# Performance work log

Hardware: AMD Instinct MI355X
Metric: run time of the kernel (lower is better)

## Reference

```python
import jax, jax.numpy as jnp
import numpy as np

N = 50000      # nodes
E = 1600000    # edges (avg degree 32)
F_IN = 256     # input feature dim
H = 128        # hidden == output size of GCN
C = 40         # num_class


def setup_inputs() -> dict:
    key = jax.random.key(0)
    ks = jax.random.split(key, 13)
    inp = {
        "features": jax.random.normal(ks[0], (N, F_IN), dtype=jnp.float32),
        "src": jax.random.randint(ks[1], (E,), 0, N, dtype=jnp.int32),
        "dst": jax.random.randint(ks[2], (E,), 0, N, dtype=jnp.int32),
        "edge_weight": jax.random.uniform(ks[3], (E,), dtype=jnp.float32),
        "y": jax.random.normal(ks[4], (N, C), dtype=jnp.float32),
        # GCN layer 1
        "W1": jax.random.normal(ks[5], (F_IN, H), dtype=jnp.float32) / np.sqrt(F_IN),
        "b1": jnp.zeros((H,), dtype=jnp.float32),
        # GCN layer 2
        "W2": jax.random.normal(ks[6], (H, H), dtype=jnp.float32) / np.sqrt(H),
        "b2": jnp.zeros((H,), dtype=jnp.float32),
        # y_fc_emb: Linear(num_class, output_size)
        "We": jax.random.normal(ks[7], (C, H), dtype=jnp.float32) / np.sqrt(C),
        "be": jnp.zeros((H,), dtype=jnp.float32),
        # y_fc: Linear(hidden*2, num_class)
        "Wf": jax.random.normal(ks[8], (2 * H, C), dtype=jnp.float32) / np.sqrt(2 * H),
        "bf": jnp.zeros((C,), dtype=jnp.float32),
    }
    return inp


def _spmm(edge_weight, src, dst, x, n):
    # (sparse adj) @ x : out[i] = sum_{(j->i)} w_ji * x[j]
    return jax.ops.segment_sum(edge_weight[:, None] * x[src], dst, num_segments=n)


def reference(features, src, dst, edge_weight, y, W1, b1, W2, b2, We, be, Wf, bf):
    n = features.shape[0]
    # F.normalize: L2 row-normalize with eps=1e-12 clamp
    norm = jnp.maximum(jnp.linalg.norm(features, axis=1, keepdims=True), 1e-12)
    x = features / norm
    # GCN layer 1: relu(adj @ (x @ W1) + b1)   (dropout = 0)
    h = jax.nn.relu(_spmm(edge_weight, src, dst, x @ W1, n) + b1)
    # GCN layer 2: adj @ (h @ W2) + b2
    h = _spmm(edge_weight, src, dst, h @ W2, n) + b2
    # label embedding + head
    y_emb = y @ We + be
    logits = jnp.concatenate([y_emb, h], axis=1) @ Wf + bf
    return jax.nn.softmax(logits, axis=-1)
```

## Files before the change

### kernel.cpp

```cpp
#include <hip/hip_runtime.h>
#include <hip/hip_bf16.h>
#include <hip/hip_fp16.h>
#include <cstdint>
#include <cstddef>
#include <cmath>

#define F_IN 256
#define HDIM 128
#define CCLS 40
#define NBMAX 1024
#define EPB 8192
#define CAP 4096

typedef short bf16x8 __attribute__((ext_vector_type(8)));
typedef float f32x4 __attribute__((ext_vector_type(4)));

__device__ inline unsigned pkbf(float a, float b) {
  __hip_bfloat162 h = __float22bfloat162_rn(make_float2(a, b));
  unsigned u;
  __builtin_memcpy(&u, &h, 4);
  return u;
}
__device__ inline unsigned short bfr(float f) {
  __hip_bfloat16 h = __float2bfloat16(f);
  unsigned short u;
  __builtin_memcpy(&u, &h, 2);
  return u;
}
__device__ inline float f16tof(unsigned short hb) {
  __half hv;
  __builtin_memcpy(&hv, &hb, 2);
  return __half2float(hv);
}
__device__ inline unsigned short ftof16(float f) {
  __half hv = __float2half(f);
  unsigned short u;
  __builtin_memcpy(&u, &hv, 2);
  return u;
}

__global__ __launch_bounds__(256) void prep_kernel(const float* __restrict__ W1,
                                                   unsigned short* __restrict__ W1T,
                                                   int* __restrict__ gcursor, int nb) {
  const int b = blockIdx.x;
  const int t = threadIdx.x;
  if (b < 128) {
    int idx = b * 256 + t;
    int nr = idx >> 8, k = idx & 255;
    W1T[idx] = bfr(W1[k * 128 + nr]);
  } else {
    for (int i = t; i < nb; i += 256) gcursor[i] = 0;
  }
}

__global__ __launch_bounds__(256) void scatter_gemm1(const int* __restrict__ src,
                                                     const int* __restrict__ dst,
                                                     const float* __restrict__ w,
                                                     int* __restrict__ gcursor,
                                                     uint2* __restrict__ ews,
                                                     const float* __restrict__ X,
                                                     const unsigned short* __restrict__ W1T,
                                                     unsigned short* __restrict__ C,
                                                     const float* __restrict__ W2,
                                                     unsigned short* __restrict__ W2T,
                                                     const float* __restrict__ We,
                                                     const float* __restrict__ be,
                                                     const float* __restrict__ Wf,
                                                     const float* __restrict__ bf,
                                                     float* __restrict__ Wc,
                                                     float* __restrict__ bc,
                                                     int e, int nb, int nsb, int ngb,
                                                     int M) {
  __shared__ char smem[16 * 264 * 2];
  const int t = threadIdx.x;
  const int b = blockIdx.x;
  if (b < nsb) {
    int* hist = (int*)smem;
    int* sb   = hist + NBMAX;
    for (int i = t; i < nb; i += 256) hist[i] = 0;
    __syncthreads();
    const int b4 = b * (EPB / 4);
    int4 dv[8];
    int rk[32];
#pragma unroll
    for (int k = 0; k < 8; ++k) {
      int gi = b4 + k * 256 + t;
      int e0 = gi * 4;
      int4 d = make_int4(-1, -1, -1, -1);
      if (e0 + 3 < e) d = ((const int4*)dst)[gi];
      else if (e0 < e) {
        d.x = dst[e0];
        if (e0 + 1 < e) d.y = dst[e0 + 1];
        if (e0 + 2 < e) d.z = dst[e0 + 2];
      }
      dv[k] = d;
      rk[k * 4 + 0] = (d.x >= 0) ? atomicAdd(&hist[d.x >> 6], 1) : 0;
      rk[k * 4 + 1] = (d.y >= 0) ? atomicAdd(&hist[d.y >> 6], 1) : 0;
      rk[k * 4 + 2] = (d.z >= 0) ? atomicAdd(&hist[d.z >> 6], 1) : 0;
      rk[k * 4 + 3] = (d.w >= 0) ? atomicAdd(&hist[d.w >> 6], 1) : 0;
    }
    __syncthreads();
    for (int i = t; i < nb; i += 256) {
      int c = hist[i];
      sb[i] = i * CAP + (c ? atomicAdd(&gcursor[i], c) : 0);
    }
    __syncthreads();
#pragma unroll
    for (int k = 0; k < 8; ++k) {
      int gi = b4 + k * 256 + t;
      int e0 = gi * 4;
      if (e0 >= e) continue;
      int4 s4 = make_int4(0, 0, 0, 0);
      float4 w4 = make_float4(0.f, 0.f, 0.f, 0.f);
      if (e0 + 3 < e) { s4 = ((const int4*)src)[gi]; w4 = ((const float4*)w)[gi]; }
      else {
        s4.x = src[e0]; w4.x = w[e0];
        if (e0 + 1 < e) { s4.y = src[e0 + 1]; w4.y = w[e0 + 1]; }
        if (e0 + 2 < e) { s4.z = src[e0 + 2]; w4.z = w[e0 + 2]; }
      }
      int4 d = dv[k];
      if (d.x >= 0) ews[sb[d.x >> 6] + rk[k * 4 + 0]] =
          make_uint2(((unsigned)(d.x & 63) << 26) | (unsigned)s4.x, __float_as_uint(w4.x));
      if (d.y >= 0) ews[sb[d.y >> 6] + rk[k * 4 + 1]] =
          make_uint2(((unsigned)(d.y & 63) << 26) | (unsigned)s4.y, __float_as_uint(w4.y));
      if (d.z >= 0) ews[sb[d.z >> 6] + rk[k * 4 + 2]] =
          make_uint2(((unsigned)(d.z & 63) << 26) | (unsigned)s4.z, __float_as_uint(w4.z));
      if (d.w >= 0) ews[sb[d.w >> 6] + rk[k * 4 + 3]] =
          make_uint2(((unsigned)(d.w & 63) << 26) | (unsigned)s4.w, __float_as_uint(w4.w));
    }
  } else if (b < nsb + ngb) {
    unsigned short (*As)[264] = (unsigned short(*)[264])smem;
    const int w8 = t >> 6, l = t & 63;
    const int bm0 = (b - nsb) * 16;
    for (int rr = 0; rr < 4; ++rr) {
      int row = w8 * 4 + rr;
      int grow = bm0 + row;
      const float* p = X + (size_t)(grow < M ? grow : (M - 1)) * F_IN + l * 4;
      float4 v = *(const float4*)p;
      float s = v.x * v.x + v.y * v.y + v.z * v.z + v.w * v.w;
#pragma unroll
      for (int off = 32; off; off >>= 1) s += __shfl_xor(s, off, 64);
      float inv = 1.0f / fmaxf(sqrtf(s), 1e-12f);
      *(uint2*)&As[row][l * 4] =
          make_uint2(pkbf(v.x * inv, v.y * inv), pkbf(v.z * inv, v.w * inv));
    }
    __syncthreads();
    const int ln = l & 15, quad = l >> 4;
    f32x4 acc[2];
    acc[0] = (f32x4){0.f, 0.f, 0.f, 0.f};
    acc[1] = (f32x4){0.f, 0.f, 0.f, 0.f};
#pragma unroll
    for (int k0 = 0; k0 < F_IN; k0 += 32) {
      bf16x8 af = *(const bf16x8*)&As[ln][k0 + quad * 8];
#pragma unroll
      for (int ti = 0; ti < 2; ++ti) {
        bf16x8 bfv = *(const bf16x8*)(W1T + (size_t)(w8 * 32 + ti * 16 + ln) * F_IN +
                                      k0 + quad * 8);
        acc[ti] = __builtin_amdgcn_mfma_f32_16x16x32_bf16(af, bfv, acc[ti], 0, 0, 0);
      }
    }
#pragma unroll
    for (int r = 0; r < 4; ++r) {
      int grow = bm0 + quad * 4 + r;
      if (grow < M) {
#pragma unroll
        for (int ti = 0; ti < 2; ++ti)
          C[(size_t)grow * HDIM + w8 * 32 + ti * 16 + ln] = bfr(acc[ti][r]);
      }
    }
  } else if (b < nsb + ngb + 64) {
    int idx = (b - nsb - ngb) * 256 + t;
    int nr = idx >> 7, k = idx & 127;
    W2T[idx] = bfr(W2[k * 128 + nr]);
  } else {
    int part = b - (nsb + ngb + 64);
    int lo = part * 800, hi = lo + 800;
    for (int i = lo + t; i < hi; i += 256) {
      int c = i / CCLS, j = i % CCLS;
      float s = 0.f;
      for (int f = 0; f < HDIM; ++f) s += We[c * HDIM + f] * Wf[f * CCLS + j];
      Wc[i] = s;
    }
    if (part == 0 && t < CCLS) {
      float s = bf[t];
      for (int f = 0; f < HDIM; ++f) s += be[f] * Wf[f * CCLS + t];
      bc[t] = s;
    }
  }
}

__global__ __launch_bounds__(256) void bucket_sort(const uint2* __restrict__ ews,
                                                   const int* __restrict__ gcursor,
                                                   unsigned* __restrict__ ews2,
                                                   int* __restrict__ row_off,
                                                   int* __restrict__ row_end,
                                                   int n, int nb) {
  __shared__ int cnt[256];
  __shared__ int cur[64];
  const int t = threadIdx.x;
  const int b = blockIdx.x;
  cnt[t] = 0;
  __syncthreads();
  const int base = b * CAP;
  const int c = gcursor[b];
  const int wv = t >> 6;
  for (int i = t; i < c; i += 256)
    atomicAdd(&cnt[wv * 64 + ((unsigned)ews[base + i].x >> 26)], 1);
  __syncthreads();
  if (t < 64) {
    int tot = cnt[t] + cnt[64 + t] + cnt[128 + t] + cnt[192 + t];
    int x = tot;
#pragma unroll
    for (int off = 1; off < 64; off <<= 1) {
      int y = __shfl_up(x, off, 64);
      if (t >= off) x += y;
    }
    int excl = x - tot;
    cur[t] = excl;
    int node = b * 64 + t;
    if (node < n) { row_off[node] = base + excl; row_end[node] = base + excl + tot; }
  }
  __syncthreads();
  for (int i = t; i < c; i += 256) {
    uint2 p = ews[base + i];
    int d = (unsigned)p.x >> 26;
    int pos = base + atomicAdd(&cur[d], 1);
    ews2[pos] = (p.x & 0xFFFFu) | ((unsigned)ftof16(__uint_as_float(p.y)) << 16);
  }
}

#define SPMM_PAIR(ua, ub)                                                      \
  {                                                                            \
    unsigned u = half ? (ub) : (ua);                                           \
    float wt = f16tof((unsigned short)(u >> 16));                              \
    const uint2 xv = *(const uint2*)(xin + (size_t)(u & 0xFFFFu) * HDIM + fo); \
    acc.x = fmaf(wt, __uint_as_float(xv.x << 16), acc.x);                      \
    acc.y = fmaf(wt, __uint_as_float(xv.x & 0xFFFF0000u), acc.y);              \
    acc.z = fmaf(wt, __uint_as_float(xv.y << 16), acc.z);                      \
    acc.w = fmaf(wt, __uint_as_float(xv.y & 0xFFFF0000u), acc.w);              \
  }

#define SPMM_NODE_LOOP(ep, cnt)                                                 \
  int k = 0;                                                                    \
  for (; k + 16 <= cnt; k += 16) {                                              \
    unsigned a0 = ep[k + 0], a1 = ep[k + 1], a2 = ep[k + 2], a3 = ep[k + 3];    \
    unsigned a4 = ep[k + 4], a5 = ep[k + 5], a6 = ep[k + 6], a7 = ep[k + 7];    \
    unsigned a8 = ep[k + 8], a9 = ep[k + 9], a10 = ep[k + 10], a11 = ep[k + 11];\
    unsigned a12 = ep[k + 12], a13 = ep[k + 13], a14 = ep[k + 14],              \
             a15 = ep[k + 15];                                                  \
    SPMM_PAIR(a0, a1); SPMM_PAIR(a2, a3); SPMM_PAIR(a4, a5); SPMM_PAIR(a6, a7); \
    SPMM_PAIR(a8, a9); SPMM_PAIR(a10, a11); SPMM_PAIR(a12, a13);                \
    SPMM_PAIR(a14, a15);                                                        \
  }                                                                             \
  for (; k + 8 <= cnt; k += 8) {                                                \
    unsigned a0 = ep[k + 0], a1 = ep[k + 1], a2 = ep[k + 2], a3 = ep[k + 3];    \
    unsigned a4 = ep[k + 4], a5 = ep[k + 5], a6 = ep[k + 6], a7 = ep[k + 7];    \
    SPMM_PAIR(a0, a1); SPMM_PAIR(a2, a3); SPMM_PAIR(a4, a5); SPMM_PAIR(a6, a7); \
  }                                                                             \
  for (; k < cnt; k += 2) {                                                     \
    unsigned a0 = ep[k];                                                        \
    unsigned a1 = (k + 1 < cnt) ? ep[k + 1] : 0u;                               \
    SPMM_PAIR(a0, a1);                                                          \
  }

__global__ __launch_bounds__(256) void spmm1_gemm2(const unsigned short* __restrict__ xin,
                                                   const unsigned* __restrict__ ews,
                                                   const int* __restrict__ row_off,
                                                   const int* __restrict__ row_end,
                                                   const float* __restrict__ bias,
                                                   const unsigned short* __restrict__ W2T,
                                                   unsigned short* __restrict__ C,
                                                   int n) {
  __shared__ unsigned short As[16][136];
  const int t = threadIdx.x;
  const int l = t & 63;
  const int w = t >> 6;
  const int fo = (l & 31) * 4;
  const int half = l >> 5;
  const int nb0 = blockIdx.x * 16;
#pragma unroll
  for (int j = 0; j < 4; ++j) {
    const int node = nb0 + w * 4 + j;
    if (node < n) {
      const int ue0 = __builtin_amdgcn_readfirstlane(row_off[node]);
      const int ue1 = __builtin_amdgcn_readfirstlane(row_end[node]);
      const int cnt = ue1 - ue0;
      const unsigned* ep = ews + ue0;
      float4 acc = make_float4(0.f, 0.f, 0.f, 0.f);
      SPMM_NODE_LOOP(ep, cnt)
      acc.x += __shfl_xor(acc.x, 32, 64);
      acc.y += __shfl_xor(acc.y, 32, 64);
      acc.z += __shfl_xor(acc.z, 32, 64);
      acc.w += __shfl_xor(acc.w, 32, 64);
      if (l < 32) {
        float4 bv = *(const float4*)(bias + fo);
        float r0 = fmaxf(acc.x + bv.x, 0.f), r1 = fmaxf(acc.y + bv.y, 0.f);
        float r2 = fmaxf(acc.z + bv.z, 0.f), r3 = fmaxf(acc.w + bv.w, 0.f);
        *(uint2*)&As[w * 4 + j][fo] = make_uint2(pkbf(r0, r1), pkbf(r2, r3));
      }
    }
  }
  __syncthreads();
  const int ln = l & 15, quad = l >> 4;
  f32x4 acc2[2];
  acc2[0] = (f32x4){0.f, 0.f, 0.f, 0.f};
  acc2[1] = (f32x4){0.f, 0.f, 0.f, 0.f};
#pragma unroll
  for (int k0 = 0; k0 < HDIM; k0 += 32) {
    bf16x8 af = *(const bf16x8*)&As[ln][k0 + quad * 8];
#pragma unroll
    for (int ti = 0; ti < 2; ++ti) {
      bf16x8 bfv = *(const bf16x8*)(W2T + (size_t)(w * 32 + ti * 16 + ln) * HDIM +
                                    k0 + quad * 8);
      acc2[ti] = __builtin_amdgcn_mfma_f32_16x16x32_bf16(af, bfv, acc2[ti], 0, 0, 0);
    }
  }
#pragma unroll
  for (int r = 0; r < 4; ++r) {
    int grow = nb0 + quad * 4 + r;
    if (grow < n) {
#pragma unroll
      for (int ti = 0; ti < 2; ++ti)
        C[(size_t)grow * HDIM + w * 32 + ti * 16 + ln] = bfr(acc2[ti][r]);
    }
  }
}

__global__ __launch_bounds__(256) void spmm_f32(const unsigned short* __restrict__ xin,
                                                const unsigned* __restrict__ ews,
                                                const int* __restrict__ row_off,
                                                const int* __restrict__ row_end,
                                                const float* __restrict__ bias,
                                                float* __restrict__ outp, int n) {
  const int t = threadIdx.x;
  const int l = t & 63;
  const int node = blockIdx.x * 4 + (t >> 6);
  if (node >= n) return;
  const int ue0 = __builtin_amdgcn_readfirstlane(row_off[node]);
  const int ue1 = __builtin_amdgcn_readfirstlane(row_end[node]);
  const int cnt = ue1 - ue0;
  const unsigned* ep = ews + ue0;
  const int fo = (l & 31) * 4;
  const int half = l >> 5;
  float4 acc = make_float4(0.f, 0.f, 0.f, 0.f);
  SPMM_NODE_LOOP(ep, cnt)
  acc.x += __shfl_xor(acc.x, 32, 64);
  acc.y += __shfl_xor(acc.y, 32, 64);
  acc.z += __shfl_xor(acc.z, 32, 64);
  acc.w += __shfl_xor(acc.w, 32, 64);
  if (l < 32) {
    float4 bv = *(const float4*)(bias + fo);
    *(float4*)(outp + (size_t)node * HDIM + fo) =
        make_float4(acc.x + bv.x, acc.y + bv.y, acc.z + bv.z, acc.w + bv.w);
  }
}

__global__ __launch_bounds__(256) void head_kernel(const float* __restrict__ y,
                                                   const float* __restrict__ h2,
                                                   const float* __restrict__ Wc,
                                                   const float* __restrict__ bc,
                                                   const float* __restrict__ Wf,
                                                   float* __restrict__ out, int n) {
  __shared__ float sW[169 * CCLS];
  const int t = threadIdx.x;
  for (int i = t; i < 400; i += 256) ((float4*)sW)[i] = ((const float4*)Wc)[i];
  for (int i = t; i < 1280; i += 256)
    ((float4*)(sW + CCLS * CCLS))[i] = ((const float4*)(Wf + HDIM * CCLS))[i];
  if (t < 10) ((float4*)(sW + 168 * CCLS))[t] = ((const float4*)bc)[t];
  __syncthreads();

  const int node = blockIdx.x * 256 + t;
  const int nc = node < n ? node : n - 1;
  const float* zy = y + (size_t)nc * CCLS;
  const float* zh = h2 + (size_t)nc * HDIM;

  float acc[40];
#pragma unroll
  for (int cq = 0; cq < 10; ++cq) {
    float4 b4 = *(const float4*)&sW[168 * CCLS + cq * 4];
    acc[cq * 4 + 0] = b4.x; acc[cq * 4 + 1] = b4.y;
    acc[cq * 4 + 2] = b4.z; acc[cq * 4 + 3] = b4.w;
  }

#pragma unroll 2
  for (int kc = 0; kc < 10; ++kc) {
    float4 zv = *(const float4*)(zy + kc * 4);
    float zj[4] = {zv.x, zv.y, zv.z, zv.w};
#pragma unroll
    for (int j = 0; j < 4; ++j) {
      const float* wr = sW + (kc * 4 + j) * CCLS;
#pragma unroll
      for (int cq = 0; cq < 10; ++cq) {
        float4 w4 = *(const float4*)(wr + cq * 4);
        acc[cq * 4 + 0] = fmaf(zj[j], w4.x, acc[cq * 4 + 0]);
        acc[cq * 4 + 1] = fmaf(zj[j], w4.y, acc[cq * 4 + 1]);
        acc[cq * 4 + 2] = fmaf(zj[j], w4.z, acc[cq * 4 + 2]);
        acc[cq * 4 + 3] = fmaf(zj[j], w4.w, acc[cq * 4 + 3]);
      }
    }
  }
#pragma unroll 2
  for (int kc = 0; kc < 32; ++kc) {
    float4 zv = *(const float4*)(zh + kc * 4);
    float zj[4] = {zv.x, zv.y, zv.z, zv.w};
#pragma unroll
    for (int j = 0; j < 4; ++j) {
      const float* wr = sW + (40 + kc * 4 + j) * CCLS;
#pragma unroll
      for (int cq = 0; cq < 10; ++cq) {
        float4 w4 = *(const float4*)(wr + cq * 4);
        acc[cq * 4 + 0] = fmaf(zj[j], w4.x, acc[cq * 4 + 0]);
        acc[cq * 4 + 1] = fmaf(zj[j], w4.y, acc[cq * 4 + 1]);
        acc[cq * 4 + 2] = fmaf(zj[j], w4.z, acc[cq * 4 + 2]);
        acc[cq * 4 + 3] = fmaf(zj[j], w4.w, acc[cq * 4 + 3]);
      }
    }
  }

  float m = acc[0];
#pragma unroll
  for (int c = 1; c < 40; ++c) m = fmaxf(m, acc[c]);
  float sum = 0.f;
#pragma unroll
  for (int c = 0; c < 40; ++c) { acc[c] = __expf(acc[c] - m); sum += acc[c]; }
  float inv = 1.0f / sum;
  if (node < n) {
    float* op = out + (size_t)node * CCLS;
#pragma unroll
    for (int cq = 0; cq < 10; ++cq) {
      float4 o = make_float4(acc[cq * 4 + 0] * inv, acc[cq * 4 + 1] * inv,
                             acc[cq * 4 + 2] * inv, acc[cq * 4 + 3] * inv);
      *(float4*)(op + cq * 4) = o;
    }
  }
}

extern "C" void kernel_launch(void* const* d_in, const int* in_sizes, int n_in,
                              void* d_out, int out_size, void* d_ws, size_t ws_size,
                              hipStream_t stream) {
  (void)n_in; (void)out_size; (void)ws_size;
  const float* features = (const float*)d_in[0];
  const int*   src      = (const int*)d_in[1];
  const int*   dst      = (const int*)d_in[2];
  const float* ew       = (const float*)d_in[3];
  const float* y        = (const float*)d_in[4];
  const float* W1       = (const float*)d_in[5];
  const float* b1       = (const float*)d_in[6];
  const float* W2       = (const float*)d_in[7];
  const float* b2       = (const float*)d_in[8];
  const float* We       = (const float*)d_in[9];
  const float* be       = (const float*)d_in[10];
  const float* Wf       = (const float*)d_in[11];
  const float* bf       = (const float*)d_in[12];
  float* out = (float*)d_out;

  const int n = in_sizes[0] / F_IN;
  const int e = in_sizes[1];
  const int nb = (n + 63) >> 6;

  char* w = (char*)d_ws;
  auto take = [&](size_t bytes) {
    char* p = w;
    w += (bytes + 255) & ~(size_t)255;
    return p;
  };
  int*   gcursor  = (int*)take((size_t)nb * 4);
  int*   row_off  = (int*)take((size_t)n * 4);
  int*   row_end  = (int*)take((size_t)n * 4);
  uint2* ews      = (uint2*)take((size_t)nb * CAP * 8);
  unsigned* ews2  = (unsigned*)take((size_t)nb * CAP * 4);
  unsigned short* bufH1  = (unsigned short*)take((size_t)n * HDIM * 2);
  unsigned short* bufH2  = (unsigned short*)take((size_t)n * HDIM * 2);
  float* bufS     = (float*)take((size_t)n * HDIM * 4);
  unsigned short* W1T = (unsigned short*)take((size_t)HDIM * F_IN * 2);
  unsigned short* W2T = (unsigned short*)take((size_t)HDIM * HDIM * 2);
  float* Wc       = (float*)take(CCLS * CCLS * 4);
  float* bc       = (float*)take(CCLS * 4);

  const int nsb = (e + EPB - 1) / EPB;
  const int ngb = (n + 15) / 16;

  prep_kernel<<<129, 256, 0, stream>>>(W1, W1T, gcursor, nb);
  scatter_gemm1<<<nsb + ngb + 64 + 2, 256, 0, stream>>>(
      src, dst, ew, gcursor, ews, features, W1T, bufH1,
      W2, W2T, We, be, Wf, bf, Wc, bc, e, nb, nsb, ngb, n);
  bucket_sort<<<nb, 256, 0, stream>>>(ews, gcursor, ews2, row_off, row_end, n, nb);

  spmm1_gemm2<<<(n + 15) / 16, 256, 0, stream>>>(bufH1, ews2, row_off, row_end, b1,
                                                 W2T, bufH2, n);
  spmm_f32<<<(n + 3) / 4, 256, 0, stream>>>(bufH2, ews2, row_off, row_end, b2, bufS, n);
  head_kernel<<<(n + 255) / 256, 256, 0, stream>>>(y, bufS, Wc, bc, Wf, out, n);
}
```

Baseline: 325.3 us.

## Replace global bucket cursor atomics with per-block fixed slot regions

The edge scatter no longer does a two-pass histogram with global atomicAdd cursors. Each scatter block writes its edges straight into a private fixed-size slot region per destination bucket and records its per-bucket counts. bucket_sort then prefix-sums those counts across scatter blocks and uses a binary search to gather the edges. This removes the global atomics, two barriers and the gcursor zeroing. In exchange it roughly doubles the staging buffer, makes the gather reads more scattered, and assumes no block puts more than 40 edges in one bucket and that there are at most 256 scatter blocks.

```diff
diff --git a/kernel.cpp b/kernel.cpp
--- a/kernel.cpp
+++ b/kernel.cpp
@@ -11,6 +11,7 @@
 #define NBMAX 1024
 #define EPB 8192
 #define CAP 4096
+#define SLOTS_PB 40
 
 typedef short bf16x8 __attribute__((ext_vector_type(8)));
 typedef float f32x4 __attribute__((ext_vector_type(4)));
@@ -40,23 +41,16 @@
 }
 
 __global__ __launch_bounds__(256) void prep_kernel(const float* __restrict__ W1,
-                                                   unsigned short* __restrict__ W1T,
-                                                   int* __restrict__ gcursor, int nb) {
-  const int b = blockIdx.x;
-  const int t = threadIdx.x;
-  if (b < 128) {
-    int idx = b * 256 + t;
-    int nr = idx >> 8, k = idx & 255;
-    W1T[idx] = bfr(W1[k * 128 + nr]);
-  } else {
-    for (int i = t; i < nb; i += 256) gcursor[i] = 0;
-  }
+                                                   unsigned short* __restrict__ W1T) {
+  int idx = blockIdx.x * 256 + threadIdx.x;
+  int nr = idx >> 8, k = idx & 255;
+  W1T[idx] = bfr(W1[k * 128 + nr]);
 }
 
 __global__ __launch_bounds__(256) void scatter_gemm1(const int* __restrict__ src,
                                                      const int* __restrict__ dst,
                                                      const float* __restrict__ w,
-                                                     int* __restrict__ gcursor,
+                                                     int* __restrict__ cnt,
                                                      uint2* __restrict__ ews,
                                                      const float* __restrict__ X,
                                                      const unsigned short* __restrict__ W1T,
@@ -76,58 +70,41 @@
   const int b = blockIdx.x;
   if (b < nsb) {
     int* hist = (int*)smem;
-    int* sb   = hist + NBMAX;
     for (int i = t; i < nb; i += 256) hist[i] = 0;
     __syncthreads();
     const int b4 = b * (EPB / 4);
-    int4 dv[8];
-    int rk[32];
-#pragma unroll
-    for (int k = 0; k < 8; ++k) {
-      int gi = b4 + k * 256 + t;
-      int e0 = gi * 4;
-      int4 d = make_int4(-1, -1, -1, -1);
-      if (e0 + 3 < e) d = ((const int4*)dst)[gi];
-      else if (e0 < e) {
-        d.x = dst[e0];
-        if (e0 + 1 < e) d.y = dst[e0 + 1];
-        if (e0 + 2 < e) d.z = dst[e0 + 2];
-      }
-      dv[k] = d;
-      rk[k * 4 + 0] = (d.x >= 0) ? atomicAdd(&hist[d.x >> 6], 1) : 0;
-      rk[k * 4 + 1] = (d.y >= 0) ? atomicAdd(&hist[d.y >> 6], 1) : 0;
-      rk[k * 4 + 2] = (d.z >= 0) ? atomicAdd(&hist[d.z >> 6], 1) : 0;
-      rk[k * 4 + 3] = (d.w >= 0) ? atomicAdd(&hist[d.w >> 6], 1) : 0;
-    }
-    __syncthreads();
-    for (int i = t; i < nb; i += 256) {
-      int c = hist[i];
-      sb[i] = i * CAP + (c ? atomicAdd(&gcursor[i], c) : 0);
-    }
-    __syncthreads();
 #pragma unroll
     for (int k = 0; k < 8; ++k) {
       int gi = b4 + k * 256 + t;
       int e0 = gi * 4;
       if (e0 >= e) continue;
+      int4 d = make_int4(-1, -1, -1, -1);
       int4 s4 = make_int4(0, 0, 0, 0);
       float4 w4 = make_float4(0.f, 0.f, 0.f, 0.f);
-      if (e0 + 3 < e) { s4 = ((const int4*)src)[gi]; w4 = ((const float4*)w)[gi]; }
-      else {
-        s4.x = src[e0]; w4.x = w[e0];
-        if (e0 + 1 < e) { s4.y = src[e0 + 1]; w4.y = w[e0 + 1]; }
-        if (e0 + 2 < e) { s4.z = src[e0 + 2]; w4.z = w[e0 + 2]; }
-      }
-      int4 d = dv[k];
-      if (d.x >= 0) ews[sb[d.x >> 6] + rk[k * 4 + 0]] =
-          make_uint2(((unsigned)(d.x & 63) << 26) | (unsigned)s4.x, __float_as_uint(w4.x));
-      if (d.y >= 0) ews[sb[d.y >> 6] + rk[k * 4 + 1]] =
-          make_uint2(((unsigned)(d.y & 63) << 26) | (unsigned)s4.y, __float_as_uint(w4.y));
-      if (d.z >= 0) ews[sb[d.z >> 6] + rk[k * 4 + 2]] =
-          make_uint2(((unsigned)(d.z & 63) << 26) | (unsigned)s4.z, __float_as_uint(w4.z));
-      if (d.w >= 0) ews[sb[d.w >> 6] + rk[k * 4 + 3]] =
-          make_uint2(((unsigned)(d.w & 63) << 26) | (unsigned)s4.w, __float_as_uint(w4.w));
-    }
+      if (e0 + 3 < e) {
+        d = ((const int4*)dst)[gi];
+        s4 = ((const int4*)src)[gi];
+        w4 = ((const float4*)w)[gi];
+      } else {
+        d.x = dst[e0]; s4.x = src[e0]; w4.x = w[e0];
+        if (e0 + 1 < e) { d.y = dst[e0 + 1]; s4.y = src[e0 + 1]; w4.y = w[e0 + 1]; }
+        if (e0 + 2 < e) { d.z = dst[e0 + 2]; s4.z = src[e0 + 2]; w4.z = w[e0 + 2]; }
+      }
+      if (d.x >= 0) { int bb = d.x >> 6; int r = atomicAdd(&hist[bb], 1);
+        ews[((size_t)bb * nsb + b) * SLOTS_PB + r] =
+            make_uint2(((unsigned)(d.x & 63) << 26) | (unsigned)s4.x, __float_as_uint(w4.x)); }
+      if (d.y >= 0) { int bb = d.y >> 6; int r = atomicAdd(&hist[bb], 1);
+        ews[((size_t)bb * nsb + b) * SLOTS_PB + r] =
+            make_uint2(((unsigned)(d.y & 63) << 26) | (unsigned)s4.y, __float_as_uint(w4.y)); }
+      if (d.z >= 0) { int bb = d.z >> 6; int r = atomicAdd(&hist[bb], 1);
+        ews[((size_t)bb * nsb + b) * SLOTS_PB + r] =
+            make_uint2(((unsigned)(d.z & 63) << 26) | (unsigned)s4.z, __float_as_uint(w4.z)); }
+      if (d.w >= 0) { int bb = d.w >> 6; int r = atomicAdd(&hist[bb], 1);
+        ews[((size_t)bb * nsb + b) * SLOTS_PB + r] =
+            make_uint2(((unsigned)(d.w & 63) << 26) | (unsigned)s4.w, __float_as_uint(w4.w)); }
+    }
+    __syncthreads();
+    for (int i = t; i < nb; i += 256) cnt[(size_t)b * nb + i] = hist[i];
   } else if (b < nsb + ngb) {
     unsigned short (*As)[264] = (unsigned short(*)[264])smem;
     const int w8 = t >> 6, l = t & 63;
@@ -190,25 +167,42 @@
 }
 
 __global__ __launch_bounds__(256) void bucket_sort(const uint2* __restrict__ ews,
-                                                   const int* __restrict__ gcursor,
+                                                   const int* __restrict__ cnt,
                                                    unsigned* __restrict__ ews2,
                                                    int* __restrict__ row_off,
                                                    int* __restrict__ row_end,
-                                                   int n, int nb) {
-  __shared__ int cnt[256];
+                                                   int n, int nb, int nsb) {
+  __shared__ int sc[256];
+  __shared__ int cc[256];
+  __shared__ int c64[256];
   __shared__ int cur[64];
   const int t = threadIdx.x;
   const int b = blockIdx.x;
-  cnt[t] = 0;
+  int c = (t < nsb) ? cnt[(size_t)t * nb + b] : 0;
+  cc[t] = c;
+  sc[t] = c;
+  c64[t] = 0;
   __syncthreads();
-  const int base = b * CAP;
-  const int c = gcursor[b];
+  for (int off = 1; off < 256; off <<= 1) {
+    int x = sc[t];
+    int y = (t >= off) ? sc[t - off] : 0;
+    __syncthreads();
+    sc[t] = x + y;
+    __syncthreads();
+  }
+  const int total = sc[255];
+  const size_t cbase = (size_t)b * nsb * SLOTS_PB;
   const int wv = t >> 6;
-  for (int i = t; i < c; i += 256)
-    atomicAdd(&cnt[wv * 64 + ((unsigned)ews[base + i].x >> 26)], 1);
+  for (int p = t; p < total; p += 256) {
+    int lo = 0, hi = nsb - 1;
+    while (lo < hi) { int mid = (lo + hi) >> 1; if (sc[mid] > p) hi = mid; else lo = mid + 1; }
+    int ii = p - (sc[lo] - cc[lo]);
+    uint2 r = ews[cbase + (size_t)lo * SLOTS_PB + ii];
+    atomicAdd(&c64[wv * 64 + ((unsigned)r.x >> 26)], 1);
+  }
   __syncthreads();
   if (t < 64) {
-    int tot = cnt[t] + cnt[64 + t] + cnt[128 + t] + cnt[192 + t];
+    int tot = c64[t] + c64[64 + t] + c64[128 + t] + c64[192 + t];
     int x = tot;
 #pragma unroll
     for (int off = 1; off < 64; off <<= 1) {
@@ -218,14 +212,17 @@
     int excl = x - tot;
     cur[t] = excl;
     int node = b * 64 + t;
-    if (node < n) { row_off[node] = base + excl; row_end[node] = base + excl + tot; }
+    if (node < n) { row_off[node] = b * CAP + excl; row_end[node] = b * CAP + excl + tot; }
   }
   __syncthreads();
-  for (int i = t; i < c; i += 256) {
-    uint2 p = ews[base + i];
-    int d = (unsigned)p.x >> 26;
-    int pos = base + atomicAdd(&cur[d], 1);
-    ews2[pos] = (p.x & 0xFFFFu) | ((unsigned)ftof16(__uint_as_float(p.y)) << 16);
+  for (int p = t; p < total; p += 256) {
+    int lo = 0, hi = nsb - 1;
+    while (lo < hi) { int mid = (lo + hi) >> 1; if (sc[mid] > p) hi = mid; else lo = mid + 1; }
+    int ii = p - (sc[lo] - cc[lo]);
+    uint2 r = ews[cbase + (size_t)lo * SLOTS_PB + ii];
+    int tag = (unsigned)r.x >> 26;
+    int pos = atomicAdd(&cur[tag], 1);
+    ews2[b * CAP + pos] = (r.x & 0xFFFFu) | ((unsigned)ftof16(__uint_as_float(r.y)) << 16);
   }
 }
 
@@ -457,6 +454,8 @@
   const int n = in_sizes[0] / F_IN;
   const int e = in_sizes[1];
   const int nb = (n + 63) >> 6;
+  const int nsb = (e + EPB - 1) / EPB;
+  const int ngb = (n + 15) / 16;
 
   char* w = (char*)d_ws;
   auto take = [&](size_t bytes) {
@@ -464,10 +463,10 @@
     w += (bytes + 255) & ~(size_t)255;
     return p;
   };
-  int*   gcursor  = (int*)take((size_t)nb * 4);
+  int*   cnt      = (int*)take((size_t)nsb * nb * 4);
   int*   row_off  = (int*)take((size_t)n * 4);
   int*   row_end  = (int*)take((size_t)n * 4);
-  uint2* ews      = (uint2*)take((size_t)nb * CAP * 8);
+  uint2* ews      = (uint2*)take((size_t)nb * nsb * SLOTS_PB * 8);
   unsigned* ews2  = (unsigned*)take((size_t)nb * CAP * 4);
   unsigned short* bufH1  = (unsigned short*)take((size_t)n * HDIM * 2);
   unsigned short* bufH2  = (unsigned short*)take((size_t)n * HDIM * 2);
@@ -477,14 +476,11 @@
   float* Wc       = (float*)take(CCLS * CCLS * 4);
   float* bc       = (float*)take(CCLS * 4);
 
-  const int nsb = (e + EPB - 1) / EPB;
-  const int ngb = (n + 15) / 16;
-
-  prep_kernel<<<129, 256, 0, stream>>>(W1, W1T, gcursor, nb);
+  prep_kernel<<<128, 256, 0, stream>>>(W1, W1T);
   scatter_gemm1<<<nsb + ngb + 64 + 2, 256, 0, stream>>>(
-      src, dst, ew, gcursor, ews, features, W1T, bufH1,
+      src, dst, ew, cnt, ews, features, W1T, bufH1,
       W2, W2T, We, be, Wf, bf, Wc, bc, e, nb, nsb, ngb, n);
-  bucket_sort<<<nb, 256, 0, stream>>>(ews, gcursor, ews2, row_off, row_end, n, nb);
+  bucket_sort<<<nb, 256, 0, stream>>>(ews, cnt, ews2, row_off, row_end, n, nb, nsb);
 
   spmm1_gemm2<<<(n + 15) / 16, 256, 0, stream>>>(bufH1, ews2, row_off, row_end, b1,
                                                  W2T, bufH2, n);
```

Measured after the change: 344.2 us. 5.8% more time.

## Replace fixed-capacity edge buckets with exact counted offsets via prepass histogram

Applied to the files above, without the earlier changes.

Adds a global histogram pass over dst in the prep kernel so each 64-node bucket's exact edge count is known. Every scatter block then computes exclusive prefix offsets, which gives a compact edge array instead of fixed CAP-sized buckets. Bucket_sort finds its start by summing the preceding counts. This removes the CAP overflow assumption and makes the edge lists contiguous and smaller, at the cost of an extra pass over dst, a per-block prefix scan, and a memset.

```diff
diff --git a/kernel.cpp b/kernel.cpp
--- a/kernel.cpp
+++ b/kernel.cpp
@@ -9,8 +9,8 @@
 #define HDIM 128
 #define CCLS 40
 #define NBMAX 1024
+#define EPB_H 16384
 #define EPB 8192
-#define CAP 4096
 
 typedef short bf16x8 __attribute__((ext_vector_type(8)));
 typedef float f32x4 __attribute__((ext_vector_type(4)));
@@ -41,7 +41,9 @@
 
 __global__ __launch_bounds__(256) void prep_kernel(const float* __restrict__ W1,
                                                    unsigned short* __restrict__ W1T,
-                                                   int* __restrict__ gcursor, int nb) {
+                                                   const int* __restrict__ dst,
+                                                   int* __restrict__ gcount,
+                                                   int e, int nb) {
   const int b = blockIdx.x;
   const int t = threadIdx.x;
   if (b < 128) {
@@ -49,13 +51,36 @@
     int nr = idx >> 8, k = idx & 255;
     W1T[idx] = bfr(W1[k * 128 + nr]);
   } else {
-    for (int i = t; i < nb; i += 256) gcursor[i] = 0;
+    __shared__ int h[NBMAX];
+    for (int i = t; i < nb; i += 256) h[i] = 0;
+    __syncthreads();
+    int b4 = (b - 128) * (EPB_H / 4);
+#pragma unroll
+    for (int k = 0; k < EPB_H / 1024; ++k) {
+      int gi = b4 + k * 256 + t;
+      int e0 = gi * 4;
+      int4 d = make_int4(-1, -1, -1, -1);
+      if (e0 + 3 < e) d = ((const int4*)dst)[gi];
+      else if (e0 < e) {
+        d.x = dst[e0];
+        if (e0 + 1 < e) d.y = dst[e0 + 1];
+        if (e0 + 2 < e) d.z = dst[e0 + 2];
+      }
+      if (d.x >= 0) atomicAdd(&h[d.x >> 6], 1);
+      if (d.y >= 0) atomicAdd(&h[d.y >> 6], 1);
+      if (d.z >= 0) atomicAdd(&h[d.z >> 6], 1);
+      if (d.w >= 0) atomicAdd(&h[d.w >> 6], 1);
+    }
+    __syncthreads();
+    for (int i = t; i < nb; i += 256)
+      if (h[i]) atomicAdd(&gcount[i], h[i]);
   }
 }
 
 __global__ __launch_bounds__(256) void scatter_gemm1(const int* __restrict__ src,
                                                      const int* __restrict__ dst,
                                                      const float* __restrict__ w,
+                                                     const int* __restrict__ gcount,
                                                      int* __restrict__ gcursor,
                                                      uint2* __restrict__ ews,
                                                      const float* __restrict__ X,
@@ -71,62 +96,90 @@
                                                      float* __restrict__ bc,
                                                      int e, int nb, int nsb, int ngb,
                                                      int M) {
-  __shared__ char smem[16 * 264 * 2];
+  __shared__ char smem[3 * NBMAX * 4 + 256 * 4];
   const int t = threadIdx.x;
   const int b = blockIdx.x;
   if (b < nsb) {
     int* hist = (int*)smem;
     int* sb   = hist + NBMAX;
-    for (int i = t; i < nb; i += 256) hist[i] = 0;
+    int* lcur = sb + NBMAX;
+    int* part = lcur + NBMAX;
+    for (int i = t; i < nb; i += 256) { hist[i] = 0; lcur[i] = 0; }
     __syncthreads();
     const int b4 = b * (EPB / 4);
-    int4 dv[8];
-    int rk[32];
-#pragma unroll
-    for (int k = 0; k < 8; ++k) {
-      int gi = b4 + k * 256 + t;
-      int e0 = gi * 4;
-      int4 d = make_int4(-1, -1, -1, -1);
-      if (e0 + 3 < e) d = ((const int4*)dst)[gi];
-      else if (e0 < e) {
-        d.x = dst[e0];
-        if (e0 + 1 < e) d.y = dst[e0 + 1];
-        if (e0 + 2 < e) d.z = dst[e0 + 2];
-      }
-      dv[k] = d;
-      rk[k * 4 + 0] = (d.x >= 0) ? atomicAdd(&hist[d.x >> 6], 1) : 0;
-      rk[k * 4 + 1] = (d.y >= 0) ? atomicAdd(&hist[d.y >> 6], 1) : 0;
-      rk[k * 4 + 2] = (d.z >= 0) ? atomicAdd(&hist[d.z >> 6], 1) : 0;
-      rk[k * 4 + 3] = (d.w >= 0) ? atomicAdd(&hist[d.w >> 6], 1) : 0;
-    }
-    __syncthreads();
-    for (int i = t; i < nb; i += 256) {
-      int c = hist[i];
-      sb[i] = i * CAP + (c ? atomicAdd(&gcursor[i], c) : 0);
-    }
-    __syncthreads();
 #pragma unroll
     for (int k = 0; k < 8; ++k) {
       int gi = b4 + k * 256 + t;
       int e0 = gi * 4;
       if (e0 >= e) continue;
+      int4 d = make_int4(-1, -1, -1, -1);
+      if (e0 + 3 < e) d = ((const int4*)dst)[gi];
+      else {
+        d.x = dst[e0];
+        if (e0 + 1 < e) d.y = dst[e0 + 1];
+        if (e0 + 2 < e) d.z = dst[e0 + 2];
+      }
+      if (d.x >= 0) atomicAdd(&hist[d.x >> 6], 1);
+      if (d.y >= 0) atomicAdd(&hist[d.y >> 6], 1);
+      if (d.z >= 0) atomicAdd(&hist[d.z >> 6], 1);
+      if (d.w >= 0) atomicAdd(&hist[d.w >> 6], 1);
+    }
+    __syncthreads();
+    int v[4];
+    int s = 0;
+#pragma unroll
+    for (int k = 0; k < 4; ++k) {
+      int i = t * 4 + k;
+      v[k] = (i < nb) ? gcount[i] : 0;
+      s += v[k];
+    }
+    part[t] = s;
+    __syncthreads();
+    for (int off = 1; off < 256; off <<= 1) {
+      int x = part[t];
+      if (t >= off) x += part[t - off];
+      __syncthreads();
+      part[t] = x;
+      __syncthreads();
+    }
+    int run = (t == 0) ? 0 : part[t - 1];
+#pragma unroll
+    for (int k = 0; k < 4; ++k) {
+      int i = t * 4 + k;
+      if (i < nb) sb[i] = run;
+      run += v[k];
+    }
+    __syncthreads();
+    for (int i = t; i < nb; i += 256) {
+      int c = hist[i];
+      sb[i] = sb[i] + (c ? atomicAdd(&gcursor[i], c) : 0);
+    }
+    __syncthreads();
+#pragma unroll
+    for (int k = 0; k < 8; ++k) {
+      int gi = b4 + k * 256 + t;
+      int e0 = gi * 4;
+      if (e0 >= e) continue;
+      int4 d = make_int4(-1, -1, -1, -1);
       int4 s4 = make_int4(0, 0, 0, 0);
       float4 w4 = make_float4(0.f, 0.f, 0.f, 0.f);
-      if (e0 + 3 < e) { s4 = ((const int4*)src)[gi]; w4 = ((const float4*)w)[gi]; }
-      else {
-        s4.x = src[e0]; w4.x = w[e0];
-        if (e0 + 1 < e) { s4.y = src[e0 + 1]; w4.y = w[e0 + 1]; }
-        if (e0 + 2 < e) { s4.z = src[e0 + 2]; w4.z = w[e0 + 2]; }
-      }
-      int4 d = dv[k];
-      if (d.x >= 0) ews[sb[d.x >> 6] + rk[k * 4 + 0]] =
-          make_uint2(((unsigned)(d.x & 63) << 26) | (unsigned)s4.x, __float_as_uint(w4.x));
-      if (d.y >= 0) ews[sb[d.y >> 6] + rk[k * 4 + 1]] =
-          make_uint2(((unsigned)(d.y & 63) << 26) | (unsigned)s4.y, __float_as_uint(w4.y));
-      if (d.z >= 0) ews[sb[d.z >> 6] + rk[k * 4 + 2]] =
-          make_uint2(((unsigned)(d.z & 63) << 26) | (unsigned)s4.z, __float_as_uint(w4.z));
-      if (d.w >= 0) ews[sb[d.w >> 6] + rk[k * 4 + 3]] =
-          make_uint2(((unsigned)(d.w & 63) << 26) | (unsigned)s4.w, __float_as_uint(w4.w));
+      if (e0 + 3 < e) {
+        d = ((const int4*)dst)[gi];
+        s4 = ((const int4*)src)[gi];
+        w4 = ((const float4*)w)[gi];
+      } else {
+        d.x = dst[e0]; s4.x = src[e0]; w4.x = w[e0];
+        if (e0 + 1 < e) { d.y = dst[e0 + 1]; s4.y = src[e0 + 1]; w4.y = w[e0 + 1]; }
+        if (e0 + 2 < e) { d.z = dst[e0 + 2]; s4.z = src[e0 + 2]; w4.z = w[e0 + 2]; }
+      }
+      if (d.x >= 0) { int bb = d.x >> 6; int r = atomicAdd(&lcur[bb], 1);
+        ews[sb[bb] + r] = make_uint2(((unsigned)(d.x & 63) << 26) | (unsigned)s4.x, __float_as_uint(w4.x)); }
+      if (d.y >= 0) { int bb = d.y >> 6; int r = atomicAdd(&lcur[bb], 1);
+        ews[sb[bb] + r] = make_uint2(((unsigned)(d.y & 63) << 26) | (unsigned)s4.y, __float_as_uint(w4.y)); }
+      if (d.z >= 0) { int bb = d.z >> 6; int r = atomicAdd(&lcur[bb], 1);
+        ews[sb[bb] + r] = make_uint2(((unsigned)(d.z & 63) << 26) | (unsigned)s4.z, __float_as_uint(w4.z)); }
+      if (d.w >= 0) { int bb = d.w >> 6; int r = atomicAdd(&lcur[bb], 1);
+        ews[sb[bb] + r] = make_uint2(((unsigned)(d.w & 63) << 26) | (unsigned)s4.w, __float_as_uint(w4.w)); }
     }
   } else if (b < nsb + ngb) {
     unsigned short (*As)[264] = (unsigned short(*)[264])smem;
@@ -190,22 +243,28 @@
 }
 
 __global__ __launch_bounds__(256) void bucket_sort(const uint2* __restrict__ ews,
-                                                   const int* __restrict__ gcursor,
+                                                   const int* __restrict__ gcount,
                                                    unsigned* __restrict__ ews2,
                                                    int* __restrict__ row_off,
                                                    int* __restrict__ row_end,
                                                    int n, int nb) {
   __shared__ int cnt[256];
   __shared__ int cur[64];
+  __shared__ int sred[4];
   const int t = threadIdx.x;
   const int b = blockIdx.x;
+  int partial = 0;
+  for (int i = t; i < b; i += 256) partial += gcount[i];
+#pragma unroll
+  for (int off = 32; off; off >>= 1) partial += __shfl_xor(partial, off, 64);
+  if ((t & 63) == 0) sred[t >> 6] = partial;
   cnt[t] = 0;
   __syncthreads();
-  const int base = b * CAP;
-  const int c = gcursor[b];
+  const int e0 = sred[0] + sred[1] + sred[2] + sred[3];
+  const int e1 = e0 + gcount[b];
   const int wv = t >> 6;
-  for (int i = t; i < c; i += 256)
-    atomicAdd(&cnt[wv * 64 + ((unsigned)ews[base + i].x >> 26)], 1);
+  for (int i = e0 + t; i < e1; i += 256)
+    atomicAdd(&cnt[wv * 64 + ((unsigned)ews[i].x >> 26)], 1);
   __syncthreads();
   if (t < 64) {
     int tot = cnt[t] + cnt[64 + t] + cnt[128 + t] + cnt[192 + t];
@@ -218,13 +277,13 @@
     int excl = x - tot;
     cur[t] = excl;
     int node = b * 64 + t;
-    if (node < n) { row_off[node] = base + excl; row_end[node] = base + excl + tot; }
+    if (node < n) { row_off[node] = e0 + excl; row_end[node] = e0 + excl + tot; }
   }
   __syncthreads();
-  for (int i = t; i < c; i += 256) {
-    uint2 p = ews[base + i];
+  for (int i = e0 + t; i < e1; i += 256) {
+    uint2 p = ews[i];
     int d = (unsigned)p.x >> 26;
-    int pos = base + atomicAdd(&cur[d], 1);
+    int pos = e0 + atomicAdd(&cur[d], 1);
     ews2[pos] = (p.x & 0xFFFFu) | ((unsigned)ftof16(__uint_as_float(p.y)) << 16);
   }
 }
@@ -457,6 +516,9 @@
   const int n = in_sizes[0] / F_IN;
   const int e = in_sizes[1];
   const int nb = (n + 63) >> 6;
+  const int hb  = (e + EPB_H - 1) / EPB_H;
+  const int nsb = (e + EPB - 1) / EPB;
+  const int ngb = (n + 15) / 16;
 
   char* w = (char*)d_ws;
   auto take = [&](size_t bytes) {
@@ -464,11 +526,13 @@
     w += (bytes + 255) & ~(size_t)255;
     return p;
   };
-  int*   gcursor  = (int*)take((size_t)nb * 4);
+  int*   gz       = (int*)take((size_t)2 * nb * 4);
+  int*   gcount   = gz;
+  int*   gcursor  = gz + nb;
   int*   row_off  = (int*)take((size_t)n * 4);
   int*   row_end  = (int*)take((size_t)n * 4);
-  uint2* ews      = (uint2*)take((size_t)nb * CAP * 8);
-  unsigned* ews2  = (unsigned*)take((size_t)nb * CAP * 4);
+  uint2* ews      = (uint2*)take((size_t)e * 8);
+  unsigned* ews2  = (unsigned*)take((size_t)(e + 16) * 4);
   unsigned short* bufH1  = (unsigned short*)take((size_t)n * HDIM * 2);
   unsigned short* bufH2  = (unsigned short*)take((size_t)n * HDIM * 2);
   float* bufS     = (float*)take((size_t)n * HDIM * 4);
@@ -477,14 +541,12 @@
   float* Wc       = (float*)take(CCLS * CCLS * 4);
   float* bc       = (float*)take(CCLS * 4);
 
-  const int nsb = (e + EPB - 1) / EPB;
-  const int ngb = (n + 15) / 16;
-
-  prep_kernel<<<129, 256, 0, stream>>>(W1, W1T, gcursor, nb);
+  hipMemsetAsync(gz, 0, (size_t)2 * nb * 4, stream);
+  prep_kernel<<<128 + hb, 256, 0, stream>>>(W1, W1T, dst, gcount, e, nb);
   scatter_gemm1<<<nsb + ngb + 64 + 2, 256, 0, stream>>>(
-      src, dst, ew, gcursor, ews, features, W1T, bufH1,
+      src, dst, ew, gcount, gcursor, ews, features, W1T, bufH1,
       W2, W2T, We, be, Wf, bf, Wc, bc, e, nb, nsb, ngb, n);
-  bucket_sort<<<nb, 256, 0, stream>>>(ews, gcursor, ews2, row_off, row_end, n, nb);
+  bucket_sort<<<nb, 256, 0, stream>>>(ews, gcount, ews2, row_off, row_end, n, nb);
 
   spmm1_gemm2<<<(n + 15) / 16, 256, 0, stream>>>(bufH1, ews2, row_off, row_end, b1,
                                                  W2T, bufH2, n);
```

Result: slower. 332.4 us (+2.2%).
